# Kernel tuning notes

Measured on AMD Instinct MI355X. Metric: run time of the kernel, lower is better.

Reference implementation:

```python
import jax, jax.numpy as jnp
import numpy as np

BN_EPS = 1e-5
NORM_EPS = 1e-6


def _nearest_resize(m, H, W):
    # torch F.interpolate(mode='nearest'): idx = floor(i * in/out)
    B, C, h, w = m.shape
    iy = (jnp.arange(H) * h) // H
    ix = (jnp.arange(W) * w) // W
    return m[:, :, iy][:, :, :, ix]


def _distance_transform(m_s):
    # Euclidean distance of every pixel to nearest foreground pixel (mask>0.5),
    # normalized per-sample to [0,1]; all-background samples -> ones map.
    B, _, H, W = m_s.shape
    HW = H * W
    yy, xx = jnp.meshgrid(jnp.arange(H, dtype=jnp.float32),
                          jnp.arange(W, dtype=jnp.float32), indexing='ij')
    ys, xs = yy.reshape(-1), xx.reshape(-1)
    # shared [HW, HW] pairwise squared distances (same for all batch elems)
    D2 = (ys[:, None] - ys[None, :]) ** 2 + (xs[:, None] - xs[None, :]) ** 2
    fg = m_s.reshape(B, HW) > 0.5                                  # [B, HW]
    min_d2 = jnp.min(jnp.where(fg[:, None, :], D2[None], jnp.inf), axis=-1)  # [B, HW]
    has_fg = fg.any(axis=1, keepdims=True)
    dist = jnp.where(has_fg, jnp.sqrt(min_d2), 1.0)
    mx = dist.max(axis=1, keepdims=True)
    dist = dist / (mx + NORM_EPS)
    return dist.reshape(B, 1, H, W)


def _forward(f_s, supp_feat_bin, support_mask, w_fusion, gamma, beta):
    B, C, H, W = f_s.shape
    m_s = _nearest_resize(support_mask, H, W)
    attn = jax.nn.sigmoid(jnp.sum(f_s * supp_feat_bin, axis=1, keepdims=True))  # [B,1,H,W]
    f_w = f_s * attn
    dist = _distance_transform(m_s)
    fusion_in = jnp.concatenate([f_s, supp_feat_bin, f_w, dist], axis=1)  # [B,3C+1,H,W]
    y = jnp.einsum('oc,bchw->bohw', w_fusion, fusion_in)  # 1x1 conv, no bias
    # BatchNorm2d in training mode: biased batch stats over (B,H,W)
    mean = y.mean(axis=(0, 2, 3))
    var = y.var(axis=(0, 2, 3))
    yn = (y - mean[None, :, None, None]) * jax.lax.rsqrt(var[None, :, None, None] + BN_EPS)
    return jax.nn.relu(yn * gamma[None, :, None, None] + beta[None, :, None, None])


def setup_inputs() -> dict:
    key = jax.random.key(0)
    k1, k2, k3, k4 = jax.random.split(key, 4)
    B, C, H, W = 8, 256, 64, 64
    Hm, Wm = 256, 256
    return {
        'f_s': jax.random.normal(k1, (B, C, H, W), dtype=jnp.float32),
        'supp_feat_bin': jax.random.normal(k2, (B, C, H, W), dtype=jnp.float32),
        'support_mask': jax.random.uniform(k3, (B, 1, Hm, Wm), dtype=jnp.float32),
        'w_fusion': jax.random.normal(k4, (C, 3 * C + 1), dtype=jnp.float32) * 0.02,
        'gamma': jnp.ones((C,), dtype=jnp.float32),
        'beta': jnp.zeros((C,), dtype=jnp.float32),
    }


def reference(f_s, supp_feat_bin, support_mask, w_fusion, gamma, beta):
    return _forward(f_s, supp_feat_bin, support_mask, w_fusion, gamma, beta)
```

## Files before the change

kernel.cpp:

```cpp
#include <hip/hip_runtime.h>
#include <math.h>

#define C_IN   256
#define HW_    4096
#define KW_    769
#define NPIX_BN 32768.0f

typedef short bf16x8 __attribute__((ext_vector_type(8)));
typedef float f32x4  __attribute__((ext_vector_type(4)));
typedef unsigned short u16x4 __attribute__((ext_vector_type(4)));

__device__ inline unsigned short f2bf(float x){
    unsigned u = __float_as_uint(x);
    u += 0x7fffu + ((u >> 16) & 1u);
    return (unsigned short)(u >> 16);
}

__global__ __launch_bounds__(256) void prep_w(
    const float* __restrict__ w, unsigned short* __restrict__ wp)
{
    int idx = blockIdx.x * 256 + threadIdx.x;
    int j  = idx & 7;
    int o  = (idx >> 3) & 255;
    int t2 = idx >> 11;
    int kq = t2 & 3, ks = (t2 >> 2) & 7, m = t2 >> 5;
    int c  = m * 256 + ks * 32 + kq * 8 + j;
    wp[idx] = f2bf(w[(size_t)o * KW_ + c]);
}

__global__ __launch_bounds__(1024) void dist_kernel(
    const float* __restrict__ mask, float* __restrict__ dist_raw,
    unsigned* __restrict__ dmax)
{
    __shared__ float2 fg[4096];
    __shared__ int cnt;
    __shared__ float wmax[16];
    int b = blockIdx.x, tile = blockIdx.y;
    int t = threadIdx.x, lane = t & 63;
    if (t == 0) cnt = 0;
    __syncthreads();
    const float* mb = mask + (size_t)b * 65536;
    #pragma unroll
    for (int r = 0; r < 4; ++r) {
        int pp = r * 1024 + t;
        int i = pp >> 6, j = pp & 63;
        bool pred = mb[i * 1024 + j * 4] > 0.5f;
        unsigned long long bal = __ballot(pred);
        int base = 0;
        if (lane == 0) base = atomicAdd(&cnt, __popcll(bal));
        base = __shfl(base, 0, 64);
        if (pred)
            fg[base + __popcll(bal & ((1ull << lane) - 1ull))] =
                make_float2((float)i, (float)j);
    }
    __syncthreads();
    int nfg = cnt;
    int pix = tile * 256 + (t >> 2);
    int q = t & 3;
    float py = (float)(pix >> 6), px = (float)(pix & 63);
    float m = 3.4e38f;
    for (int it = q; it < nfg; it += 4) {
        float dy = py - fg[it].x;
        float dx = px - fg[it].y;
        m = fminf(m, dy * dy + dx * dx);
    }
    m = fminf(m, __shfl_xor(m, 1, 64));
    m = fminf(m, __shfl_xor(m, 2, 64));
    float d = (nfg == 0) ? 1.0f : sqrtf(m);
    if (q == 0) dist_raw[b * HW_ + pix] = d;
    float mm = d;
    #pragma unroll
    for (int off = 1; off < 64; off <<= 1)
        mm = fmaxf(mm, __shfl_xor(mm, off, 64));
    if (lane == 0) wmax[t >> 6] = mm;
    __syncthreads();
    if (t == 0) {
        float M = wmax[0];
        #pragma unroll
        for (int i = 1; i < 16; ++i) M = fmaxf(M, wmax[i]);
        atomicMax(dmax + b, __float_as_uint(M));
    }
}

__global__ __launch_bounds__(256, 2) void gemm_kernel(
    const float* __restrict__ f_s, const float* __restrict__ sfb,
    const float* __restrict__ w, const unsigned short* __restrict__ wprep,
    const float* __restrict__ dist_raw, const unsigned* __restrict__ dmax,
    float* __restrict__ y, float* __restrict__ gsum, float* __restrict__ gsumsq)
{
    __shared__ unsigned short Lf[2][2048], Ls[2][2048];
    __shared__ float attn_sm[4][64];
    __shared__ float attn_fin[64];
    __shared__ float red[2][64][2];

    int bx = blockIdx.x;
    int ot = bx & 1, nt = bx >> 1;
    int oBase = ot * 128;
    int nBase = nt * 64;
    int b = nBase >> 12, pBase = nBase & 4095;
    int t = threadIdx.x;
    int lane = t & 63, g = t >> 6;
    int wo = g >> 1, wn = g & 1;
    int l15 = lane & 15, kq = lane >> 4;

    const float* fB = f_s + (size_t)b * C_IN * HW_ + pBase + lane;
    const float* sB = sfb + (size_t)b * C_IN * HW_ + pBase + lane;

    f32x4 acc[3][4][2];
    #pragma unroll
    for (int m = 0; m < 3; ++m)
        #pragma unroll
        for (int fo = 0; fo < 4; ++fo)
            #pragma unroll
            for (int fn = 0; fn < 2; ++fn)
                acc[m][fo][fn] = (f32x4){0.f, 0.f, 0.f, 0.f};

    float ap = 0.f;
    const bf16x8* WP = (const bf16x8*)wprep;

    float fv[8], sv[8];
    #pragma unroll
    for (int j = 0; j < 8; ++j) {
        fv[j] = fB[(size_t)(g * 8 + j) * HW_];
        sv[j] = sB[(size_t)(g * 8 + j) * HW_];
    }

    #pragma unroll
    for (int ks = 0; ks < 8; ++ks) {
        int cur = ks & 1;
        #pragma unroll
        for (int j = 0; j < 8; ++j) ap += fv[j] * sv[j];
        #pragma unroll
        for (int q = 0; q < 2; ++q) {
            u16x4 pf, ps;
            #pragma unroll
            for (int jj = 0; jj < 4; ++jj) {
                pf[jj] = f2bf(fv[q * 4 + jj]);
                ps[jj] = f2bf(sv[q * 4 + jj]);
            }
            ((u16x4*)Lf[cur])[(g * 64 + lane) * 2 + q] = pf;
            ((u16x4*)Ls[cur])[(g * 64 + lane) * 2 + q] = ps;
        }
        __syncthreads();
        if (ks < 7) {
            #pragma unroll
            for (int j = 0; j < 8; ++j) {
                fv[j] = fB[(size_t)((ks + 1) * 32 + g * 8 + j) * HW_];
                sv[j] = sB[(size_t)((ks + 1) * 32 + g * 8 + j) * HW_];
            }
        }
        const bf16x8* BFr = (const bf16x8*)Lf[cur];
        const bf16x8* BSr = (const bf16x8*)Ls[cur];
        bf16x8 bf0 = BFr[kq * 64 + wn * 32 + l15];
        bf16x8 bf1 = BFr[kq * 64 + wn * 32 + 16 + l15];
        bf16x8 bs0 = BSr[kq * 64 + wn * 32 + l15];
        bf16x8 bs1 = BSr[kq * 64 + wn * 32 + 16 + l15];
        #pragma unroll
        for (int fo = 0; fo < 4; ++fo) {
            int o = oBase + wo * 64 + fo * 16 + l15;
            bf16x8 a1 = WP[((0 * 8 + ks) * 4 + kq) * 256 + o];
            bf16x8 a2 = WP[((1 * 8 + ks) * 4 + kq) * 256 + o];
            bf16x8 a3 = WP[((2 * 8 + ks) * 4 + kq) * 256 + o];
            acc[0][fo][0] = __builtin_amdgcn_mfma_f32_16x16x32_bf16(a1, bf0, acc[0][fo][0], 0, 0, 0);
            acc[0][fo][1] = __builtin_amdgcn_mfma_f32_16x16x32_bf16(a1, bf1, acc[0][fo][1], 0, 0, 0);
            acc[1][fo][0] = __builtin_amdgcn_mfma_f32_16x16x32_bf16(a2, bs0, acc[1][fo][0], 0, 0, 0);
            acc[1][fo][1] = __builtin_amdgcn_mfma_f32_16x16x32_bf16(a2, bs1, acc[1][fo][1], 0, 0, 0);
            acc[2][fo][0] = __builtin_amdgcn_mfma_f32_16x16x32_bf16(a3, bf0, acc[2][fo][0], 0, 0, 0);
            acc[2][fo][1] = __builtin_amdgcn_mfma_f32_16x16x32_bf16(a3, bf1, acc[2][fo][1], 0, 0, 0);
        }
    }

    __syncthreads();
    attn_sm[g][lane] = ap;
    __syncthreads();
    if (t < 64) {
        float a = attn_sm[0][t] + attn_sm[1][t] + attn_sm[2][t] + attn_sm[3][t];
        attn_fin[t] = 1.f / (1.f + __expf(-a));
    }
    __syncthreads();

    float dinv = 1.0f / (__uint_as_float(dmax[b]) + 1e-6f);
    const float* dR = dist_raw + b * HW_ + pBase;
    float at[2], dn[2];
    #pragma unroll
    for (int fn = 0; fn < 2; ++fn) {
        int nb = wn * 32 + fn * 16 + l15;
        at[fn] = attn_fin[nb];
        dn[fn] = dR[nb] * dinv;
    }
    float s_acc[4][4], ss_acc[4][4];
    #pragma unroll
    for (int fo = 0; fo < 4; ++fo) {
        #pragma unroll
        for (int r = 0; r < 4; ++r) {
            int o = oBase + wo * 64 + fo * 16 + kq * 4 + r;
            float wd = w[(size_t)o * KW_ + 768];
            float s = 0.f, ss = 0.f;
            #pragma unroll
            for (int fn = 0; fn < 2; ++fn) {
                float v = acc[0][fo][fn][r] + acc[1][fo][fn][r]
                        + at[fn] * acc[2][fo][fn][r] + wd * dn[fn];
                int nb = wn * 32 + fn * 16 + l15;
                y[((size_t)b * C_IN + o) * HW_ + pBase + nb] = v;
                s += v; ss += v * v;
            }
            s_acc[fo][r] = s; ss_acc[fo][r] = ss;
        }
    }
    #pragma unroll
    for (int m = 8; m; m >>= 1) {
        #pragma unroll
        for (int fo = 0; fo < 4; ++fo)
            #pragma unroll
            for (int r = 0; r < 4; ++r) {
                s_acc[fo][r]  += __shfl_xor(s_acc[fo][r],  m, 64);
                ss_acc[fo][r] += __shfl_xor(ss_acc[fo][r], m, 64);
            }
    }
    if (wn == 1 && l15 == 0) {
        #pragma unroll
        for (int fo = 0; fo < 4; ++fo)
            #pragma unroll
            for (int r = 0; r < 4; ++r) {
                int ol = fo * 16 + kq * 4 + r;
                red[wo][ol][0] = s_acc[fo][r];
                red[wo][ol][1] = ss_acc[fo][r];
            }
    }
    __syncthreads();
    if (wn == 0 && l15 == 0) {
        #pragma unroll
        for (int fo = 0; fo < 4; ++fo)
            #pragma unroll
            for (int r = 0; r < 4; ++r) {
                int ol = fo * 16 + kq * 4 + r;
                int o = oBase + wo * 64 + ol;
                atomicAdd(&gsum[o],   s_acc[fo][r]  + red[wo][ol][0]);
                atomicAdd(&gsumsq[o], ss_acc[fo][r] + red[wo][ol][1]);
            }
    }
}

__global__ __launch_bounds__(256) void bn_kernel(
    const float* __restrict__ gsum, const float* __restrict__ gsumsq,
    const float* __restrict__ gamma, const float* __restrict__ beta,
    float* __restrict__ y)
{
    int bo = blockIdx.x;
    int o = bo & 255;
    float mean = gsum[o] * (1.0f / NPIX_BN);
    float var  = gsumsq[o] * (1.0f / NPIX_BN) - mean * mean;
    float sc = gamma[o] * rsqrtf(var + 1e-5f);
    float sh = beta[o] - mean * sc;
    float4* p = (float4*)(y + (size_t)bo * HW_);
    int t = threadIdx.x;
    #pragma unroll
    for (int r = 0; r < 4; ++r) {
        float4 v = p[r * 256 + t];
        v.x = fmaxf(v.x * sc + sh, 0.f);
        v.y = fmaxf(v.y * sc + sh, 0.f);
        v.z = fmaxf(v.z * sc + sh, 0.f);
        v.w = fmaxf(v.w * sc + sh, 0.f);
        p[r * 256 + t] = v;
    }
}

extern "C" void kernel_launch(void* const* d_in, const int* in_sizes, int n_in,
                              void* d_out, int out_size, void* d_ws, size_t ws_size,
                              hipStream_t stream)
{
    const float* f_s   = (const float*)d_in[0];
    const float* sfb   = (const float*)d_in[1];
    const float* mask  = (const float*)d_in[2];
    const float* w     = (const float*)d_in[3];
    const float* gamma = (const float*)d_in[4];
    const float* beta  = (const float*)d_in[5];
    float* out = (float*)d_out;
    float* ws  = (float*)d_ws;

    float*          dist_raw = ws;
    unsigned*       dmax     = (unsigned*)(ws + 32768);
    float*          gsum     = ws + 32784;
    float*          gsumsq   = ws + 33040;
    unsigned short* wprep    = (unsigned short*)(ws + 33296);

    hipMemsetAsync(ws + 32768, 0, (33296 - 32768) * 4, stream);

    prep_w<<<768, 256, 0, stream>>>(w, wprep);
    dist_kernel<<<dim3(8, 16), 1024, 0, stream>>>(mask, dist_raw, dmax);
    gemm_kernel<<<1024, 256, 0, stream>>>(f_s, sfb, w, wprep, dist_raw, dmax,
                                          out, gsum, gsumsq);
    bn_kernel<<<2048, 256, 0, stream>>>(gsum, gsumsq, gamma, beta, out);
}
```

Baseline: 245.5 us.

## Pre-convert activations to packed bf16 and store GEMM output in bf16

Adds a conv_kernel that reads f_s and supp_feat_bin once, computes the sigmoid attention, and writes both as packed bf16 planes laid out for MFMA fragment loads. The GEMM then loads its B fragments straight from global memory with no LDS staging or barriers, and stops computing attention itself. The GEMM intermediate is stored as bf16 and expanded in the BN pass, which halves that round-trip traffic. The cost is an extra kernel plus an extra write and read of the bf16 activations, and bf16 rounding of the pre-BN values.

Result: slower. 291.7 us (+18.8%).

```diff
diff --git a/kernel.cpp b/kernel.cpp
--- a/kernel.cpp
+++ b/kernel.cpp
@@ -8,12 +8,15 @@
 
 typedef short bf16x8 __attribute__((ext_vector_type(8)));
 typedef float f32x4  __attribute__((ext_vector_type(4)));
-typedef unsigned short u16x4 __attribute__((ext_vector_type(4)));
+typedef unsigned short u16x8 __attribute__((ext_vector_type(8)));
 
 __device__ inline unsigned short f2bf(float x){
     unsigned u = __float_as_uint(x);
     u += 0x7fffu + ((u >> 16) & 1u);
     return (unsigned short)(u >> 16);
+}
+__device__ inline float bf2f(unsigned short h){
+    return __uint_as_float(((unsigned)h) << 16);
 }
 
 __global__ __launch_bounds__(256) void prep_w(
@@ -26,6 +29,57 @@
     int kq = t2 & 3, ks = (t2 >> 2) & 7, m = t2 >> 5;
     int c  = m * 256 + ks * 32 + kq * 8 + j;
     wp[idx] = f2bf(w[(size_t)o * KW_ + c]);
+}
+
+__global__ __launch_bounds__(256) void conv_kernel(
+    const float* __restrict__ f_s, const float* __restrict__ sfb,
+    unsigned short* __restrict__ xf, unsigned short* __restrict__ xs,
+    float* __restrict__ attn)
+{
+    __shared__ float red[4][64];
+    int blk = blockIdx.x;
+    int t = threadIdx.x, lane = t & 63, g = t >> 6;
+    int b = blk >> 6;
+    int p = (blk & 63) * 64 + lane;
+    const float* fB = f_s + (size_t)b * C_IN * HW_ + p;
+    const float* sB = sfb + (size_t)b * C_IN * HW_ + p;
+    u16x8* XF = (u16x8*)xf;
+    u16x8* XS = (u16x8*)xs;
+
+    float ap = 0.f;
+    float fv[8], sv[8], fv2[8], sv2[8];
+    #pragma unroll
+    for (int j = 0; j < 8; ++j) {
+        fv[j] = fB[(size_t)(g * 8 + j) * HW_];
+        sv[j] = sB[(size_t)(g * 8 + j) * HW_];
+    }
+    for (int ks = 0; ks < 8; ++ks) {
+        if (ks < 7) {
+            #pragma unroll
+            for (int j = 0; j < 8; ++j) {
+                fv2[j] = fB[(size_t)((ks + 1) * 32 + g * 8 + j) * HW_];
+                sv2[j] = sB[(size_t)((ks + 1) * 32 + g * 8 + j) * HW_];
+            }
+        }
+        u16x8 pf, ps;
+        #pragma unroll
+        for (int j = 0; j < 8; ++j) {
+            ap += fv[j] * sv[j];
+            pf[j] = f2bf(fv[j]);
+            ps[j] = f2bf(sv[j]);
+        }
+        int plane = (b * 8 + ks) * 4 + g;
+        XF[(size_t)plane * HW_ + p] = pf;
+        XS[(size_t)plane * HW_ + p] = ps;
+        #pragma unroll
+        for (int j = 0; j < 8; ++j) { fv[j] = fv2[j]; sv[j] = sv2[j]; }
+    }
+    red[g][lane] = ap;
+    __syncthreads();
+    if (t < 64) {
+        float a = red[0][t] + red[1][t] + red[2][t] + red[3][t];
+        attn[blk * 64 + t] = 1.f / (1.f + __expf(-a));
+    }
 }
 
 __global__ __launch_bounds__(1024) void dist_kernel(
@@ -59,6 +113,7 @@
     int q = t & 3;
     float py = (float)(pix >> 6), px = (float)(pix & 63);
     float m = 3.4e38f;
+    #pragma unroll 4
     for (int it = q; it < nfg; it += 4) {
         float dy = py - fg[it].x;
         float dx = px - fg[it].y;
@@ -82,29 +137,27 @@
     }
 }
 
-__global__ __launch_bounds__(256, 2) void gemm_kernel(
-    const float* __restrict__ f_s, const float* __restrict__ sfb,
-    const float* __restrict__ w, const unsigned short* __restrict__ wprep,
-    const float* __restrict__ dist_raw, const unsigned* __restrict__ dmax,
-    float* __restrict__ y, float* __restrict__ gsum, float* __restrict__ gsumsq)
-{
-    __shared__ unsigned short Lf[2][2048], Ls[2][2048];
-    __shared__ float attn_sm[4][64];
-    __shared__ float attn_fin[64];
+__global__ __launch_bounds__(256) void gemm_kernel(
+    const unsigned short* __restrict__ xf, const unsigned short* __restrict__ xs,
+    const unsigned short* __restrict__ wprep, const float* __restrict__ w,
+    const float* __restrict__ attn, const float* __restrict__ dist_raw,
+    const unsigned* __restrict__ dmax,
+    unsigned short* __restrict__ ybf,
+    float* __restrict__ gsum, float* __restrict__ gsumsq)
+{
     __shared__ float red[2][64][2];
-
     int bx = blockIdx.x;
     int ot = bx & 1, nt = bx >> 1;
-    int oBase = ot * 128;
-    int nBase = nt * 64;
+    int oBase = ot * 128, nBase = nt * 64;
     int b = nBase >> 12, pBase = nBase & 4095;
-    int t = threadIdx.x;
-    int lane = t & 63, g = t >> 6;
+    int t = threadIdx.x, lane = t & 63, g = t >> 6;
     int wo = g >> 1, wn = g & 1;
     int l15 = lane & 15, kq = lane >> 4;
 
-    const float* fB = f_s + (size_t)b * C_IN * HW_ + pBase + lane;
-    const float* sB = sfb + (size_t)b * C_IN * HW_ + pBase + lane;
+    const bf16x8* XF = (const bf16x8*)xf;
+    const bf16x8* XS = (const bf16x8*)xs;
+    const bf16x8* WP = (const bf16x8*)wprep;
+    int pix = pBase + wn * 32 + l15;
 
     f32x4 acc[3][4][2];
     #pragma unroll
@@ -115,46 +168,13 @@
             for (int fn = 0; fn < 2; ++fn)
                 acc[m][fo][fn] = (f32x4){0.f, 0.f, 0.f, 0.f};
 
-    float ap = 0.f;
-    const bf16x8* WP = (const bf16x8*)wprep;
-
-    float fv[8], sv[8];
-    #pragma unroll
-    for (int j = 0; j < 8; ++j) {
-        fv[j] = fB[(size_t)(g * 8 + j) * HW_];
-        sv[j] = sB[(size_t)(g * 8 + j) * HW_];
-    }
-
-    #pragma unroll
+    #pragma unroll 4
     for (int ks = 0; ks < 8; ++ks) {
-        int cur = ks & 1;
-        #pragma unroll
-        for (int j = 0; j < 8; ++j) ap += fv[j] * sv[j];
-        #pragma unroll
-        for (int q = 0; q < 2; ++q) {
-            u16x4 pf, ps;
-            #pragma unroll
-            for (int jj = 0; jj < 4; ++jj) {
-                pf[jj] = f2bf(fv[q * 4 + jj]);
-                ps[jj] = f2bf(sv[q * 4 + jj]);
-            }
-            ((u16x4*)Lf[cur])[(g * 64 + lane) * 2 + q] = pf;
-            ((u16x4*)Ls[cur])[(g * 64 + lane) * 2 + q] = ps;
-        }
-        __syncthreads();
-        if (ks < 7) {
-            #pragma unroll
-            for (int j = 0; j < 8; ++j) {
-                fv[j] = fB[(size_t)((ks + 1) * 32 + g * 8 + j) * HW_];
-                sv[j] = sB[(size_t)((ks + 1) * 32 + g * 8 + j) * HW_];
-            }
-        }
-        const bf16x8* BFr = (const bf16x8*)Lf[cur];
-        const bf16x8* BSr = (const bf16x8*)Ls[cur];
-        bf16x8 bf0 = BFr[kq * 64 + wn * 32 + l15];
-        bf16x8 bf1 = BFr[kq * 64 + wn * 32 + 16 + l15];
-        bf16x8 bs0 = BSr[kq * 64 + wn * 32 + l15];
-        bf16x8 bs1 = BSr[kq * 64 + wn * 32 + 16 + l15];
+        int plane = (b * 8 + ks) * 4 + kq;
+        bf16x8 bf0 = XF[(size_t)plane * HW_ + pix];
+        bf16x8 bf1 = XF[(size_t)plane * HW_ + pix + 16];
+        bf16x8 bs0 = XS[(size_t)plane * HW_ + pix];
+        bf16x8 bs1 = XS[(size_t)plane * HW_ + pix + 16];
         #pragma unroll
         for (int fo = 0; fo < 4; ++fo) {
             int o = oBase + wo * 64 + fo * 16 + l15;
@@ -170,22 +190,14 @@
         }
     }
 
-    __syncthreads();
-    attn_sm[g][lane] = ap;
-    __syncthreads();
-    if (t < 64) {
-        float a = attn_sm[0][t] + attn_sm[1][t] + attn_sm[2][t] + attn_sm[3][t];
-        attn_fin[t] = 1.f / (1.f + __expf(-a));
-    }
-    __syncthreads();
-
     float dinv = 1.0f / (__uint_as_float(dmax[b]) + 1e-6f);
     const float* dR = dist_raw + b * HW_ + pBase;
+    const float* aR = attn + nBase;
     float at[2], dn[2];
     #pragma unroll
     for (int fn = 0; fn < 2; ++fn) {
         int nb = wn * 32 + fn * 16 + l15;
-        at[fn] = attn_fin[nb];
+        at[fn] = aR[nb];
         dn[fn] = dR[nb] * dinv;
     }
     float s_acc[4][4], ss_acc[4][4];
@@ -201,7 +213,7 @@
                 float v = acc[0][fo][fn][r] + acc[1][fo][fn][r]
                         + at[fn] * acc[2][fo][fn][r] + wd * dn[fn];
                 int nb = wn * 32 + fn * 16 + l15;
-                y[((size_t)b * C_IN + o) * HW_ + pBase + nb] = v;
+                ybf[((size_t)b * C_IN + o) * HW_ + pBase + nb] = f2bf(v);
                 s += v; ss += v * v;
             }
             s_acc[fo][r] = s; ss_acc[fo][r] = ss;
@@ -244,7 +256,7 @@
 __global__ __launch_bounds__(256) void bn_kernel(
     const float* __restrict__ gsum, const float* __restrict__ gsumsq,
     const float* __restrict__ gamma, const float* __restrict__ beta,
-    float* __restrict__ y)
+    const unsigned short* __restrict__ ybf, float* __restrict__ out)
 {
     int bo = blockIdx.x;
     int o = bo & 255;
@@ -252,16 +264,23 @@
     float var  = gsumsq[o] * (1.0f / NPIX_BN) - mean * mean;
     float sc = gamma[o] * rsqrtf(var + 1e-5f);
     float sh = beta[o] - mean * sc;
-    float4* p = (float4*)(y + (size_t)bo * HW_);
+    const u16x8* yp = (const u16x8*)(ybf + (size_t)bo * HW_);
+    float4* op = (float4*)(out + (size_t)bo * HW_);
     int t = threadIdx.x;
     #pragma unroll
-    for (int r = 0; r < 4; ++r) {
-        float4 v = p[r * 256 + t];
-        v.x = fmaxf(v.x * sc + sh, 0.f);
-        v.y = fmaxf(v.y * sc + sh, 0.f);
-        v.z = fmaxf(v.z * sc + sh, 0.f);
-        v.w = fmaxf(v.w * sc + sh, 0.f);
-        p[r * 256 + t] = v;
+    for (int r = 0; r < 2; ++r) {
+        u16x8 v = yp[r * 256 + t];
+        float4 lo, hi;
+        lo.x = fmaxf(bf2f(v[0]) * sc + sh, 0.f);
+        lo.y = fmaxf(bf2f(v[1]) * sc + sh, 0.f);
+        lo.z = fmaxf(bf2f(v[2]) * sc + sh, 0.f);
+        lo.w = fmaxf(bf2f(v[3]) * sc + sh, 0.f);
+        hi.x = fmaxf(bf2f(v[4]) * sc + sh, 0.f);
+        hi.y = fmaxf(bf2f(v[5]) * sc + sh, 0.f);
+        hi.z = fmaxf(bf2f(v[6]) * sc + sh, 0.f);
+        hi.w = fmaxf(bf2f(v[7]) * sc + sh, 0.f);
+        op[(r * 256 + t) * 2]     = lo;
+        op[(r * 256 + t) * 2 + 1] = hi;
     }
 }
 
@@ -282,13 +301,27 @@
     unsigned*       dmax     = (unsigned*)(ws + 32768);
     float*          gsum     = ws + 32784;
     float*          gsumsq   = ws + 33040;
-    unsigned short* wprep    = (unsigned short*)(ws + 33296);
+    float*          attn_b   = ws + 33296;
+    unsigned short* wprep    = (unsigned short*)(ws + 66064);
+
+    const size_t P1_need = ((size_t)164608 + 3 * 4194304) * 4;
+    unsigned short *xf, *xs, *ybf;
+    if (ws_size >= P1_need) {
+        xf  = (unsigned short*)(ws + 164608);
+        xs  = (unsigned short*)(ws + 164608 + 4194304);
+        ybf = (unsigned short*)(ws + 164608 + 2 * (size_t)4194304);
+    } else {
+        xf  = (unsigned short*)d_out;
+        xs  = ((unsigned short*)d_out) + 8388608;
+        ybf = (unsigned short*)(ws + 164608);
+    }
 
     hipMemsetAsync(ws + 32768, 0, (33296 - 32768) * 4, stream);
 
     prep_w<<<768, 256, 0, stream>>>(w, wprep);
+    conv_kernel<<<512, 256, 0, stream>>>(f_s, sfb, xf, xs, attn_b);
     dist_kernel<<<dim3(8, 16), 1024, 0, stream>>>(mask, dist_raw, dmax);
-    gemm_kernel<<<1024, 256, 0, stream>>>(f_s, sfb, w, wprep, dist_raw, dmax,
-                                          out, gsum, gsumsq);
-    bn_kernel<<<2048, 256, 0, stream>>>(gsum, gsumsq, gamma, beta, out);
-}
+    gemm_kernel<<<1024, 256, 0, stream>>>(xf, xs, wprep, w, attn_b, dist_raw,
+                                          dmax, ybf, gsum, gsumsq);
+    bn_kernel<<<2048, 256, 0, stream>>>(gsum, gsumsq, gamma, beta, ybf, out);
+}
```
